# Kernel optimization log

Measured on AMD Instinct MI355X. Metric: run time of the kernel, lower is better.

## Reference

```python
import jax, jax.numpy as jnp
import numpy as np

N = 50000   # nodes
E = 600000  # directed edges (self-loops added inside reference, per GCNConv default)
G = 64      # graphs in the batch
D = 128     # in_features
H = 128     # hidden_channels
C = 10      # num_classes


def setup_inputs() -> dict:
    key = jax.random.key(0)
    ks = jax.random.split(key, 9)
    x = jax.random.normal(ks[0], (N, D), dtype=jnp.float32)
    edge_index = jax.random.randint(ks[1], (2, E), 0, N, dtype=jnp.int64)
    batch = jnp.sort(jax.random.randint(ks[2], (N,), 0, G, dtype=jnp.int64))
    # GCNConv weights (glorot-ish scale) and biases; final linear layer
    W1 = jax.random.normal(ks[3], (D, H), dtype=jnp.float32) / np.sqrt(D).astype(np.float32)
    b1 = jnp.zeros((H,), dtype=jnp.float32)
    W2 = jax.random.normal(ks[4], (H, H), dtype=jnp.float32) / np.sqrt(H).astype(np.float32)
    b2 = jnp.zeros((H,), dtype=jnp.float32)
    Wlin = jax.random.normal(ks[5], (H, C), dtype=jnp.float32) / np.sqrt(H).astype(np.float32)
    blin = jnp.zeros((C,), dtype=jnp.float32)
    return {"x": x, "W1": W1, "b1": b1, "W2": W2, "b2": b2,
            "Wlin": Wlin, "blin": blin, "edge_index": edge_index, "batch": batch}


def _gcn_conv(x, W, b, row, col, norm):
    # x' = D^{-1/2}(A+I)D^{-1/2} (x W) + b ; aggregate messages from row (src) into col (dst)
    h = x @ W                                   # [N, H] dense GEMM
    msg = norm[:, None] * h[row]                # gather by source index [E+N, H]
    out = jax.ops.segment_sum(msg, col, num_segments=N)  # scatter-add to targets
    return out + b


def reference(x, W1, b1, W2, b2, Wlin, blin, edge_index, batch):
    loops = jnp.arange(N, dtype=edge_index.dtype)
    row = jnp.concatenate([edge_index[0], loops])   # sources (+ self loops)
    col = jnp.concatenate([edge_index[1], loops])   # targets (+ self loops)
    # symmetric degree normalization (degrees >= 1 thanks to self loops)
    deg = jax.ops.segment_sum(jnp.ones_like(col, dtype=jnp.float32), col, num_segments=N)
    dinv = jax.lax.rsqrt(deg)
    norm = dinv[row] * dinv[col]                    # [E+N]

    h = jax.nn.relu(_gcn_conv(x, W1, b1, row, col, norm))
    h = _gcn_conv(h, W2, b2, row, col, norm)

    # global mean pool over graphs
    sums = jax.ops.segment_sum(h, batch, num_segments=G)                       # [G, H]
    cnt = jax.ops.segment_sum(jnp.ones((N,), dtype=jnp.float32), batch, num_segments=G)
    pooled = sums / jnp.maximum(cnt, 1.0)[:, None]

    return pooled @ Wlin + blin                     # logits [G, C]
```

## Files before the change

kernel.cpp:

```cpp
#include <hip/hip_runtime.h>

#define NN 50000
#define NE 600000
#define NG 64
#define DIM 128
#define NCLS 10
#define SB 196
#define NNP 50176
#define KBLK 224
#define KCH 224
#define CAP 64
#define E2B ((NE / 2 + 255) / 256)

typedef unsigned short ushort;
typedef unsigned char uchar;
typedef __attribute__((ext_vector_type(8))) short short8;
typedef __attribute__((ext_vector_type(4))) float float4v;
typedef __attribute__((ext_vector_type(2))) float float2v;

__device__ __forceinline__ ushort f2bf(float f) {
    unsigned u = __float_as_uint(f);
    u += 0x7fff + ((u >> 16) & 1);
    return (ushort)(u >> 16);
}
__device__ __forceinline__ uchar f2fp8(float f) {
    int p = __builtin_amdgcn_cvt_pk_fp8_f32(f, f, 0, false);
    return (uchar)(p & 0xff);
}
__device__ __forceinline__ void accfp8(float* a, uint2 v) {
    float2v p0 = __builtin_amdgcn_cvt_pk_f32_fp8(v.x, false);
    float2v p1 = __builtin_amdgcn_cvt_pk_f32_fp8(v.x, true);
    float2v p2 = __builtin_amdgcn_cvt_pk_f32_fp8(v.y, false);
    float2v p3 = __builtin_amdgcn_cvt_pk_f32_fp8(v.y, true);
    a[0] += p0[0]; a[1] += p0[1]; a[2] += p1[0]; a[3] += p1[1];
    a[4] += p2[0]; a[5] += p2[1]; a[6] += p3[0]; a[7] += p3[1];
}

__global__ void k_init(int* __restrict__ cnt, const float* __restrict__ W1,
                       ushort* __restrict__ Wsw, float* __restrict__ T,
                       float* __restrict__ dinv) {
    int b = blockIdx.x, t = threadIdx.x;
    if (b < SB) {
        int i = b * 256 + t;
        if (i < NN) cnt[i] = 0;
    } else if (b < SB + 64) {
        int tid = (b - SB) * 256 + t;
        int j = tid & 7;
        int lane = (tid >> 3) & 63;
        int frag = tid >> 9;
        int nt = frag >> 2, kc = frag & 3;
        int k = kc * 32 + (lane >> 4) * 8 + j;
        int n = nt * 16 + (lane & 15);
        Wsw[tid] = f2bf(W1[k * DIM + n]);
    } else if (b < SB + 64 + 784) {
        float4* w4 = (float4*)T;
        int base = (b - SB - 64) * 256 + t;
#pragma unroll
        for (int i = 0; i < 4; ++i)
            w4[base + i * 200704] = make_float4(0.f, 0.f, 0.f, 0.f);
    } else {
        if (t < NNP - NN) dinv[NN + t] = 0.f;
    }
}

__global__ void k_fill(const int* __restrict__ row, const int* __restrict__ col,
                       int* __restrict__ cnt, int* __restrict__ ell) {
    int e = (blockIdx.x * blockDim.x + threadIdx.x) * 2;
    if (e < NE) {
        int2 r = *(const int2*)(row + e);
        int2 c = *(const int2*)(col + e);
        int p0 = atomicAdd(&cnt[c.x], 1);
        if (p0 < CAP) ell[c.x * CAP + p0] = r.x;
        int p1 = atomicAdd(&cnt[c.y], 1);
        if (p1 < CAP) ell[c.y * CAP + p1] = r.y;
    }
}

__global__ __launch_bounds__(256) void k_gemm_mfma(const float* __restrict__ Ain,
                                                   const ushort* __restrict__ Wsw,
                                                   const int* __restrict__ cnt,
                                                   uchar* __restrict__ Hs,
                                                   float* __restrict__ dinv) {
    const int t = threadIdx.x;
    const int wave = t >> 6, lane = t & 63;
    const int m = lane & 15, quad = lane >> 4;
    const int row0 = blockIdx.x * 64 + wave * 16;

    short8 bfrag[8][4];
#pragma unroll
    for (int nt = 0; nt < 8; ++nt)
#pragma unroll
        for (int kc = 0; kc < 4; ++kc)
            bfrag[nt][kc] = *(const short8*)(Wsw + ((nt * 4 + kc) * 64 + lane) * 8);

    float4v acc[8];
#pragma unroll
    for (int nt = 0; nt < 8; ++nt) acc[nt] = (float4v){0.f, 0.f, 0.f, 0.f};

    const int row = row0 + m;
    const int rclamp = row < NN ? row : NN - 1;

#pragma unroll
    for (int kc = 0; kc < 4; ++kc) {
        const float* ap = Ain + (size_t)rclamp * DIM + kc * 32 + quad * 8;
        float4 v0 = *(const float4*)ap;
        float4 v1 = *(const float4*)(ap + 4);
        union { short8 v; ushort u[8]; } tmp;
        tmp.u[0] = f2bf(v0.x); tmp.u[1] = f2bf(v0.y);
        tmp.u[2] = f2bf(v0.z); tmp.u[3] = f2bf(v0.w);
        tmp.u[4] = f2bf(v1.x); tmp.u[5] = f2bf(v1.y);
        tmp.u[6] = f2bf(v1.z); tmp.u[7] = f2bf(v1.w);
        short8 a = tmp.v;
#pragma unroll
        for (int nt = 0; nt < 8; ++nt)
            acc[nt] = __builtin_amdgcn_mfma_f32_16x16x32_bf16(a, bfrag[nt][kc], acc[nt], 0, 0, 0);
    }

#pragma unroll
    for (int reg = 0; reg < 4; ++reg) {
        int r = row0 + quad * 4 + reg;
        if (r < NN) {
            float d = rsqrtf(1.0f + (float)cnt[r]);
            if (m == 0) dinv[r] = d;
#pragma unroll
            for (int nt = 0; nt < 8; ++nt)
                Hs[(size_t)r * DIM + nt * 16 + m] = f2fp8(d * acc[nt][reg]);
        }
    }
}

__global__ __launch_bounds__(256) void k_gather_ell(const int* __restrict__ ell,
                                                    const int* __restrict__ deg,
                                                    const int* __restrict__ batch,
                                                    const float* __restrict__ bias,
                                                    const uchar* __restrict__ Hs,
                                                    float* __restrict__ T,
                                                    ushort* __restrict__ out) {
    int gt = blockIdx.x * blockDim.x + threadIdx.x;
    int node = gt >> 4, lane = gt & 15;
    if (node >= NN) return;
    const int* rowp = ell + node * CAP;
    int end = min(deg[node], CAP);
    const float d = rsqrtf(1.0f + (float)end);
    float* Trow = T + (size_t)batch[node] * NNP;
    const size_t off = (size_t)lane * 8;

    float a[8] = {0.f, 0.f, 0.f, 0.f, 0.f, 0.f, 0.f, 0.f};
    accfp8(a, *(const uint2*)(Hs + (size_t)node * DIM + off));
    if (lane == 0) atomicAdd(&Trow[node], d);

    int e = 0;
    for (; e + 8 <= end; e += 8) {
        int r0 = rowp[e], r1 = rowp[e + 1], r2 = rowp[e + 2], r3 = rowp[e + 3];
        int r4 = rowp[e + 4], r5 = rowp[e + 5], r6 = rowp[e + 6], r7 = rowp[e + 7];
        if (lane < 8) atomicAdd(&Trow[rowp[e + lane]], d);
        uint2 v0 = *(const uint2*)(Hs + (size_t)r0 * DIM + off);
        uint2 v1 = *(const uint2*)(Hs + (size_t)r1 * DIM + off);
        uint2 v2 = *(const uint2*)(Hs + (size_t)r2 * DIM + off);
        uint2 v3 = *(const uint2*)(Hs + (size_t)r3 * DIM + off);
        uint2 v4 = *(const uint2*)(Hs + (size_t)r4 * DIM + off);
        uint2 v5 = *(const uint2*)(Hs + (size_t)r5 * DIM + off);
        uint2 v6 = *(const uint2*)(Hs + (size_t)r6 * DIM + off);
        uint2 v7 = *(const uint2*)(Hs + (size_t)r7 * DIM + off);
        accfp8(a, v0); accfp8(a, v1); accfp8(a, v2); accfp8(a, v3);
        accfp8(a, v4); accfp8(a, v5); accfp8(a, v6); accfp8(a, v7);
    }
    for (; e + 4 <= end; e += 4) {
        int r0 = rowp[e], r1 = rowp[e + 1], r2 = rowp[e + 2], r3 = rowp[e + 3];
        if (lane < 4) atomicAdd(&Trow[rowp[e + lane]], d);
        uint2 v0 = *(const uint2*)(Hs + (size_t)r0 * DIM + off);
        uint2 v1 = *(const uint2*)(Hs + (size_t)r1 * DIM + off);
        uint2 v2 = *(const uint2*)(Hs + (size_t)r2 * DIM + off);
        uint2 v3 = *(const uint2*)(Hs + (size_t)r3 * DIM + off);
        accfp8(a, v0); accfp8(a, v1); accfp8(a, v2); accfp8(a, v3);
    }
    for (; e < end; ++e) {
        int r = rowp[e];
        if (lane == 0) atomicAdd(&Trow[r], d);
        accfp8(a, *(const uint2*)(Hs + (size_t)r * DIM + off));
    }

    float4 b0 = *(const float4*)(bias + off);
    float4 b1 = *(const float4*)(bias + off + 4);
    a[0] = fmaxf(fmaf(a[0], d, b0.x), 0.f); a[1] = fmaxf(fmaf(a[1], d, b0.y), 0.f);
    a[2] = fmaxf(fmaf(a[2], d, b0.z), 0.f); a[3] = fmaxf(fmaf(a[3], d, b0.w), 0.f);
    a[4] = fmaxf(fmaf(a[4], d, b1.x), 0.f); a[5] = fmaxf(fmaf(a[5], d, b1.y), 0.f);
    a[6] = fmaxf(fmaf(a[6], d, b1.z), 0.f); a[7] = fmaxf(fmaf(a[7], d, b1.w), 0.f);
    uint4 o;
    o.x = (unsigned)f2bf(a[0]) | ((unsigned)f2bf(a[1]) << 16);
    o.y = (unsigned)f2bf(a[2]) | ((unsigned)f2bf(a[3]) << 16);
    o.z = (unsigned)f2bf(a[4]) | ((unsigned)f2bf(a[5]) << 16);
    o.w = (unsigned)f2bf(a[6]) | ((unsigned)f2bf(a[7]) << 16);
    *(uint4*)(out + (size_t)node * DIM + off) = o;
}

__global__ __launch_bounds__(256) void k_pool_gemm(const float* __restrict__ T,
                                                   const float* __restrict__ dinv,
                                                   const ushort* __restrict__ A2,
                                                   float* __restrict__ partial) {
    const int t = threadIdx.x;
    const int wave = t >> 6, lane = t & 63;
    const int m = lane & 15, quad = lane >> 4;
    const int g = wave * 16 + m;
    const size_t k0 = (size_t)blockIdx.x * KCH;

    float4v acc[8];
#pragma unroll
    for (int nt = 0; nt < 8; ++nt) acc[nt] = (float4v){0.f, 0.f, 0.f, 0.f};

    for (int ks = 0; ks < KCH; ks += 32) {
        const size_t kb = k0 + ks + quad * 8;
        const float* ap = T + (size_t)g * NNP + kb;
        float4 a0 = *(const float4*)ap;
        float4 a1 = *(const float4*)(ap + 4);
        float4 d0 = *(const float4*)(dinv + kb);
        float4 d1 = *(const float4*)(dinv + kb + 4);
        union { short8 v; ushort u[8]; } af;
        af.u[0] = f2bf(a0.x * d0.x); af.u[1] = f2bf(a0.y * d0.y);
        af.u[2] = f2bf(a0.z * d0.z); af.u[3] = f2bf(a0.w * d0.w);
        af.u[4] = f2bf(a1.x * d1.x); af.u[5] = f2bf(a1.y * d1.y);
        af.u[6] = f2bf(a1.z * d1.z); af.u[7] = f2bf(a1.w * d1.w);

        const ushort* bbase = A2 + kb * DIM + m;
#pragma unroll
        for (int nt = 0; nt < 8; ++nt) {
            union { short8 v; ushort u[8]; } bf;
            const ushort* bp = bbase + nt * 16;
#pragma unroll
            for (int j = 0; j < 8; ++j) bf.u[j] = bp[(size_t)j * DIM];
            acc[nt] = __builtin_amdgcn_mfma_f32_16x16x32_bf16(af.v, bf.v, acc[nt], 0, 0, 0);
        }
    }

    float* dst = partial + (size_t)blockIdx.x * (NG * DIM);
#pragma unroll
    for (int reg = 0; reg < 4; ++reg) {
        int gg = wave * 16 + quad * 4 + reg;
#pragma unroll
        for (int nt = 0; nt < 8; ++nt)
            dst[gg * DIM + nt * 16 + m] = acc[nt][reg];
    }
}

__global__ __launch_bounds__(128) void k_final(const float* __restrict__ partial,
                                               const float* __restrict__ W2,
                                               const float* __restrict__ b2,
                                               const float* __restrict__ Wlin,
                                               const float* __restrict__ blin,
                                               const int* __restrict__ batch,
                                               float* __restrict__ out) {
    const int g = blockIdx.x;
    const int t = threadIdx.x;
    int start;
    { int a = 0, b = NN; while (a < b) { int m = (a + b) >> 1; if (batch[m] < g) a = m + 1; else b = m; } start = a; }
    int end;
    { int a = 0, b = NN; while (a < b) { int m = (a + b) >> 1; if (batch[m] < g + 1) a = m + 1; else b = m; } end = a; }
    const int cnt = end - start;

    float s = 0.f;
    for (int b = 0; b < KBLK; b += 4) {
        float s0 = partial[(size_t)(b + 0) * (NG * DIM) + g * DIM + t];
        float s1 = partial[(size_t)(b + 1) * (NG * DIM) + g * DIM + t];
        float s2 = partial[(size_t)(b + 2) * (NG * DIM) + g * DIM + t];
        float s3 = partial[(size_t)(b + 3) * (NG * DIM) + g * DIM + t];
        s += (s0 + s1) + (s2 + s3);
    }
    __shared__ float P[DIM];
    P[t] = s;
    __syncthreads();
    float acc = 0.f;
    for (int k = 0; k < DIM; ++k) acc += P[k] * W2[k * DIM + t];
    __shared__ float pooled[DIM];
    pooled[t] = (cnt > 0) ? (acc / (float)cnt + b2[t]) : 0.f;
    __syncthreads();
    if (t < NCLS) {
        float s2 = blin[t];
        for (int k = 0; k < DIM; ++k) s2 += pooled[k] * Wlin[k * NCLS + t];
        out[g * NCLS + t] = s2;
    }
}

extern "C" void kernel_launch(void* const* d_in, const int* in_sizes, int n_in,
                              void* d_out, int out_size, void* d_ws, size_t ws_size,
                              hipStream_t stream) {
    const float* x    = (const float*)d_in[0];
    const float* W1   = (const float*)d_in[1];
    const float* b1   = (const float*)d_in[2];
    const float* W2   = (const float*)d_in[3];
    const float* b2   = (const float*)d_in[4];
    const float* Wlin = (const float*)d_in[5];
    const float* blin = (const float*)d_in[6];
    const int* eidx   = (const int*)d_in[7];
    const int* batch  = (const int*)d_in[8];
    float* out = (float*)d_out;

    char* ws = (char*)d_ws;
    int*    cnt   = (int*)(ws + 0);
    float*  dinv  = (float*)(ws + 200000);
    int*    ell   = (int*)(ws + 400704);
    ushort* Wsw   = (ushort*)(ws + 13200704);
    float*  T     = (float*)(ws + 13233472);
    uchar*  Hs1   = (uchar*)(ws + 26078528);
    ushort* bufB  = (ushort*)(ws + 32478528);
    float*  poolpt= (float*)(ws + 45323584);

    const int* erow = eidx;
    const int* ecol = eidx + NE;

    k_init<<<SB + 64 + 784 + 1, 256, 0, stream>>>(cnt, W1, Wsw, T, dinv);
    k_fill<<<E2B, 256, 0, stream>>>(erow, ecol, cnt, ell);

    const int gemm_grid = (NN + 63) / 64;
    const int node_grid = (NN * 16 + 255) / 256;

    k_gemm_mfma<<<gemm_grid, 256, 0, stream>>>(x, Wsw, cnt, Hs1, dinv);
    k_gather_ell<<<node_grid, 256, 0, stream>>>(ell, cnt, batch, b1, Hs1, T, bufB);

    k_pool_gemm<<<KBLK, 256, 0, stream>>>(T, dinv, bufB, poolpt);

    k_final<<<NG, 128, 0, stream>>>(poolpt, W2, b2, Wlin, blin, batch, out);
}
```

Before: 201.5 us.

## Write gather output in MFMA-swizzled layout and reduce pool partials atomically

The gather kernel now stores its bf16 output in a tiled layout that matches the MFMA B-operand fragment order, so the pooling GEMM can load each fragment with one 16-byte vector load instead of eight strided 2-byte loads. The pooling GEMM uses smaller K chunks over more blocks and accumulates into a single [G,H] buffer with float atomics, which removes the per-block partial buffer and the reduction loop in the final kernel. The init kernel gains blocks to zero the atomic target and the padded tail of the swizzled buffer. The trade-offs are scattered 2-byte stores in the gather kernel, atomic contention on a 64x128 buffer, and a summation order that is no longer deterministic.

```diff
diff --git a/kernel.cpp b/kernel.cpp
--- a/kernel.cpp
+++ b/kernel.cpp
@@ -7,10 +7,12 @@
 #define NCLS 10
 #define SB 196
 #define NNP 50176
-#define KBLK 224
-#define KCH 224
+#define KBLK 392
+#define KCH 128
 #define CAP 64
 #define E2B ((NE / 2 + 255) / 256)
+#define NT32 (NNP / 32)
+#define BSW_TAIL_START ((size_t)(NN >> 5) * 4096)
 
 typedef unsigned short ushort;
 typedef unsigned char uchar;
@@ -38,7 +40,8 @@
 
 __global__ void k_init(int* __restrict__ cnt, const float* __restrict__ W1,
                        ushort* __restrict__ Wsw, float* __restrict__ T,
-                       float* __restrict__ dinv) {
+                       float* __restrict__ dinv, float* __restrict__ P,
+                       ushort* __restrict__ Bsw) {
     int b = blockIdx.x, t = threadIdx.x;
     if (b < SB) {
         int i = b * 256 + t;
@@ -58,8 +61,15 @@
 #pragma unroll
         for (int i = 0; i < 4; ++i)
             w4[base + i * 200704] = make_float4(0.f, 0.f, 0.f, 0.f);
+    } else if (b == SB + 64 + 784) {
+        if (t < NNP - NN) dinv[NN + t] = 0.f;
+        float4* p4 = (float4*)P;
+#pragma unroll
+        for (int i = 0; i < 8; ++i)
+            p4[i * 256 + t] = make_float4(0.f, 0.f, 0.f, 0.f);
     } else {
-        if (t < NNP - NN) dinv[NN + t] = 0.f;
+        int idx = (b - (SB + 64 + 785)) * 256 + t;
+        ((float4*)(Bsw + BSW_TAIL_START))[idx] = make_float4(0.f, 0.f, 0.f, 0.f);
     }
 }
 
@@ -186,30 +196,31 @@
     a[2] = fmaxf(fmaf(a[2], d, b0.z), 0.f); a[3] = fmaxf(fmaf(a[3], d, b0.w), 0.f);
     a[4] = fmaxf(fmaf(a[4], d, b1.x), 0.f); a[5] = fmaxf(fmaf(a[5], d, b1.y), 0.f);
     a[6] = fmaxf(fmaf(a[6], d, b1.z), 0.f); a[7] = fmaxf(fmaf(a[7], d, b1.w), 0.f);
-    uint4 o;
-    o.x = (unsigned)f2bf(a[0]) | ((unsigned)f2bf(a[1]) << 16);
-    o.y = (unsigned)f2bf(a[2]) | ((unsigned)f2bf(a[3]) << 16);
-    o.z = (unsigned)f2bf(a[4]) | ((unsigned)f2bf(a[5]) << 16);
-    o.w = (unsigned)f2bf(a[6]) | ((unsigned)f2bf(a[7]) << 16);
-    *(uint4*)(out + (size_t)node * DIM + off) = o;
+
+    ushort* bp = out + (size_t)(node >> 5) * 4096 + (size_t)(lane >> 1) * 512
+                     + (size_t)((node >> 3) & 3) * 128 + (size_t)(lane & 1) * 64
+                     + (size_t)(node & 7);
+    bp[0]  = f2bf(a[0]); bp[8]  = f2bf(a[1]); bp[16] = f2bf(a[2]); bp[24] = f2bf(a[3]);
+    bp[32] = f2bf(a[4]); bp[40] = f2bf(a[5]); bp[48] = f2bf(a[6]); bp[56] = f2bf(a[7]);
 }
 
 __global__ __launch_bounds__(256) void k_pool_gemm(const float* __restrict__ T,
                                                    const float* __restrict__ dinv,
-                                                   const ushort* __restrict__ A2,
-                                                   float* __restrict__ partial) {
+                                                   const ushort* __restrict__ Bsw,
+                                                   float* __restrict__ P) {
     const int t = threadIdx.x;
     const int wave = t >> 6, lane = t & 63;
     const int m = lane & 15, quad = lane >> 4;
     const int g = wave * 16 + m;
-    const size_t k0 = (size_t)blockIdx.x * KCH;
+    const int k0 = blockIdx.x * KCH;
 
     float4v acc[8];
 #pragma unroll
     for (int nt = 0; nt < 8; ++nt) acc[nt] = (float4v){0.f, 0.f, 0.f, 0.f};
 
-    for (int ks = 0; ks < KCH; ks += 32) {
-        const size_t kb = k0 + ks + quad * 8;
+#pragma unroll
+    for (int s = 0; s < KCH / 32; ++s) {
+        const int kb = k0 + s * 32 + quad * 8;
         const float* ap = T + (size_t)g * NNP + kb;
         float4 a0 = *(const float4*)ap;
         float4 a1 = *(const float4*)(ap + 4);
@@ -221,28 +232,25 @@
         af.u[4] = f2bf(a1.x * d1.x); af.u[5] = f2bf(a1.y * d1.y);
         af.u[6] = f2bf(a1.z * d1.z); af.u[7] = f2bf(a1.w * d1.w);
 
-        const ushort* bbase = A2 + kb * DIM + m;
+        const int t32 = (k0 >> 5) + s;
+        const ushort* bb = Bsw + (size_t)t32 * 4096 + (size_t)lane * 8;
 #pragma unroll
         for (int nt = 0; nt < 8; ++nt) {
-            union { short8 v; ushort u[8]; } bf;
-            const ushort* bp = bbase + nt * 16;
-#pragma unroll
-            for (int j = 0; j < 8; ++j) bf.u[j] = bp[(size_t)j * DIM];
-            acc[nt] = __builtin_amdgcn_mfma_f32_16x16x32_bf16(af.v, bf.v, acc[nt], 0, 0, 0);
+            short8 bv = *(const short8*)(bb + nt * 512);
+            acc[nt] = __builtin_amdgcn_mfma_f32_16x16x32_bf16(af.v, bv, acc[nt], 0, 0, 0);
         }
     }
 
-    float* dst = partial + (size_t)blockIdx.x * (NG * DIM);
 #pragma unroll
     for (int reg = 0; reg < 4; ++reg) {
         int gg = wave * 16 + quad * 4 + reg;
 #pragma unroll
         for (int nt = 0; nt < 8; ++nt)
-            dst[gg * DIM + nt * 16 + m] = acc[nt][reg];
-    }
-}
-
-__global__ __launch_bounds__(128) void k_final(const float* __restrict__ partial,
+            atomicAdd(&P[gg * DIM + nt * 16 + m], acc[nt][reg]);
+    }
+}
+
+__global__ __launch_bounds__(128) void k_final(const float* __restrict__ P,
                                                const float* __restrict__ W2,
                                                const float* __restrict__ b2,
                                                const float* __restrict__ Wlin,
@@ -257,19 +265,11 @@
     { int a = 0, b = NN; while (a < b) { int m = (a + b) >> 1; if (batch[m] < g + 1) a = m + 1; else b = m; } end = a; }
     const int cnt = end - start;
 
-    float s = 0.f;
-    for (int b = 0; b < KBLK; b += 4) {
-        float s0 = partial[(size_t)(b + 0) * (NG * DIM) + g * DIM + t];
-        float s1 = partial[(size_t)(b + 1) * (NG * DIM) + g * DIM + t];
-        float s2 = partial[(size_t)(b + 2) * (NG * DIM) + g * DIM + t];
-        float s3 = partial[(size_t)(b + 3) * (NG * DIM) + g * DIM + t];
-        s += (s0 + s1) + (s2 + s3);
-    }
-    __shared__ float P[DIM];
-    P[t] = s;
+    __shared__ float Pl[DIM];
+    Pl[t] = P[g * DIM + t];
     __syncthreads();
     float acc = 0.f;
-    for (int k = 0; k < DIM; ++k) acc += P[k] * W2[k * DIM + t];
+    for (int k = 0; k < DIM; ++k) acc += Pl[k] * W2[k * DIM + t];
     __shared__ float pooled[DIM];
     pooled[t] = (cnt > 0) ? (acc / (float)cnt + b2[t]) : 0.f;
     __syncthreads();
@@ -301,22 +301,22 @@
     ushort* Wsw   = (ushort*)(ws + 13200704);
     float*  T     = (float*)(ws + 13233472);
     uchar*  Hs1   = (uchar*)(ws + 26078528);
-    ushort* bufB  = (ushort*)(ws + 32478528);
-    float*  poolpt= (float*)(ws + 45323584);
+    ushort* Bsw   = (ushort*)(ws + 32478528);
+    float*  P     = (float*)(ws + 45323584);
 
     const int* erow = eidx;
     const int* ecol = eidx + NE;
 
-    k_init<<<SB + 64 + 784 + 1, 256, 0, stream>>>(cnt, W1, Wsw, T, dinv);
+    k_init<<<SB + 64 + 784 + 1 + 12, 256, 0, stream>>>(cnt, W1, Wsw, T, dinv, P, Bsw);
     k_fill<<<E2B, 256, 0, stream>>>(erow, ecol, cnt, ell);
 
     const int gemm_grid = (NN + 63) / 64;
     const int node_grid = (NN * 16 + 255) / 256;
 
     k_gemm_mfma<<<gemm_grid, 256, 0, stream>>>(x, Wsw, cnt, Hs1, dinv);
-    k_gather_ell<<<node_grid, 256, 0, stream>>>(ell, cnt, batch, b1, Hs1, T, bufB);
-
-    k_pool_gemm<<<KBLK, 256, 0, stream>>>(T, dinv, bufB, poolpt);
-
-    k_final<<<NG, 128, 0, stream>>>(poolpt, W2, b2, Wlin, blin, batch, out);
-}
+    k_gather_ell<<<node_grid, 256, 0, stream>>>(ell, cnt, batch, b1, Hs1, T, Bsw);
+
+    k_pool_gemm<<<KBLK, 256, 0, stream>>>(T, dinv, Bsw, P);
+
+    k_final<<<NG, 128, 0, stream>>>(P, W2, b2, Wlin, blin, batch, out);
+}
```

After: 215.2 us. 1.07x slower.
